# Performance work log

Measured on AMD Instinct MI355X. Metric: run time of the kernel, lower is better.

The kernel has to match this reference:

```python
import jax, jax.numpy as jnp
import numpy as np

N = 100000
E = 1600000
IN, HID, OUT = 128, 128, 64


def setup_inputs() -> dict:
    key = jax.random.key(0)
    k = jax.random.split(key, 8)
    x = jax.random.normal(k[0], (N, IN), dtype=jnp.float32)
    src = jax.random.randint(k[1], (E,), 0, N)
    dst = jax.random.randint(k[2], (E,), 0, N)
    # Glorot-ish init for the per-layer fc_neigh weights + biases
    W1 = jax.random.normal(k[3], (IN, HID), dtype=jnp.float32) / np.sqrt(IN)
    b1 = jnp.zeros((HID,), dtype=jnp.float32)
    W2 = jax.random.normal(k[4], (HID, OUT), dtype=jnp.float32) / np.sqrt(HID)
    b2 = jnp.zeros((OUT,), dtype=jnp.float32)
    return {"x": x, "src": src, "dst": dst, "W1": W1, "b1": b1, "W2": W2, "b2": b2}


def _sage_gcn_layer(h, src, dst, W, b):
    # DGL SAGEConv aggregator_type='gcn':
    #   neigh = sum_{u in N(v)} h_u ; h_neigh = (neigh + h_v) / (deg(v) + 1)
    #   out = h_neigh @ W + b   (fc_self unused for 'gcn')
    msg = h[src]                                              # [E, d] gather
    agg = jax.ops.segment_sum(msg, dst, num_segments=N)       # [N, d] scatter-add
    deg = jax.ops.segment_sum(jnp.ones((E,), h.dtype), dst, num_segments=N)
    h_neigh = (agg + h) / (deg[:, None] + 1.0)
    return h_neigh @ W + b


def reference(x, src, dst, W1, b1, W2, b2):
    # Dropout in eval mode (identity), as for a deterministic correctness baseline.
    h = _sage_gcn_layer(x, src, dst, W1, b1)
    h = jax.nn.relu(h)
    h = _sage_gcn_layer(h, src, dst, W2, b2)
    return h
```

## Files before the change

kernel.cpp:

```cpp
#include <hip/hip_runtime.h>

#define NN 100000
#define EE 1600000
#define FD 128
#define NBK 391
#define BCAP 5120
#define CHUNK 4096

typedef __attribute__((ext_vector_type(8))) short bf16x8;
typedef __attribute__((ext_vector_type(4))) float f32x4;

static __device__ __forceinline__ unsigned bfpack(float lo, float hi) {
  unsigned a = __float_as_uint(lo), b = __float_as_uint(hi);
  a = (a + 0x7FFFu + ((a >> 16) & 1u)) >> 16;
  b = (b + 0x7FFFu + ((b >> 16) & 1u)) >> 16;
  return a | (b << 16);
}
static __device__ __forceinline__ ushort bfround(float x) {
  unsigned u = __float_as_uint(x);
  u = (u + 0x7FFFu + ((u >> 16) & 1u)) >> 16;
  return (ushort)u;
}
static __device__ __forceinline__ float bflo(unsigned u) {
  return __uint_as_float(u << 16);
}
static __device__ __forceinline__ float bfhi(unsigned u) {
  return __uint_as_float(u & 0xFFFF0000u);
}

__global__ __launch_bounds__(256) void pass1_bin(const int* __restrict__ src,
                                                 const int* __restrict__ dst,
                                                 unsigned* __restrict__ gcur,
                                                 unsigned* __restrict__ arena) {
  __shared__ unsigned hist[NBK + 1];
  __shared__ unsigned scan[512];
  __shared__ unsigned gpos[NBK + 1];
  __shared__ unsigned sorted[CHUNK];
  int t = threadIdx.x;
  int base = blockIdx.x * CHUNK;

  hist[t] = 0;
  if (t + 256 <= NBK) hist[t + 256] = 0;
  __syncthreads();

  int dreg[16], sreg[16];
#pragma unroll
  for (int j = 0; j < 16; ++j) {
    int e = base + t + j * 256;
    if (e < EE) {
      dreg[j] = dst[e];
      sreg[j] = src[e];
      atomicAdd(&hist[dreg[j] >> 8], 1u);
    } else {
      dreg[j] = -1;
      sreg[j] = 0;
    }
  }
  __syncthreads();

  scan[t] = (t < NBK) ? hist[t] : 0;
  scan[t + 256] = (t + 256 < NBK) ? hist[t + 256] : 0;
  __syncthreads();
  for (int d = 1; d < 512; d <<= 1) {
    unsigned r0 = (t >= d) ? scan[t - d] : 0;
    unsigned r1 = ((t + 256) >= d) ? scan[t + 256 - d] : 0;
    __syncthreads();
    scan[t] += r0;
    scan[t + 256] += r1;
    __syncthreads();
  }
  unsigned c0 = (t < NBK) ? scan[t] - hist[t] : 0;
  unsigned c1 = (t + 256 < NBK) ? scan[t + 256] - hist[t + 256] : 0;
  __syncthreads();
  if (t < NBK) hist[t] = c0;
  if (t + 256 < NBK) hist[t + 256] = c1;
  __syncthreads();

#pragma unroll
  for (int j = 0; j < 16; ++j) {
    if (dreg[j] >= 0) {
      int b = dreg[j] >> 8;
      unsigned pos = atomicAdd(&hist[b], 1u);
      sorted[pos] = ((unsigned)(dreg[j] & 255) << 20) | (unsigned)sreg[j];
    }
  }
  __syncthreads();

  if (t < NBK) {
    unsigned lo = t ? scan[t - 1] : 0;
    unsigned cntb = scan[t] - lo;
    if (cntb) gpos[t] = atomicAdd(&gcur[t], cntb);
  }
  if (t + 256 < NBK) {
    unsigned lo = scan[t + 255];
    unsigned cntb = scan[t + 256] - lo;
    if (cntb) gpos[t + 256] = atomicAdd(&gcur[t + 256], cntb);
  }
  __syncthreads();

  int w = t >> 6, lane = t & 63;
  for (int b = w; b < NBK; b += 4) {
    unsigned lo = b ? scan[b - 1] : 0;
    unsigned cntb = scan[b] - lo;
    if (!cntb) continue;
    unsigned gp = gpos[b];
    if (gp >= BCAP) continue;
    unsigned lim = min(gp + cntb, (unsigned)BCAP) - gp;
    for (unsigned i = lane; i < lim; i += 64)
      arena[(size_t)b * BCAP + gp + i] = sorted[lo + i];
  }
}

__global__ __launch_bounds__(256) void bscan_kernel(const unsigned* __restrict__ gcur,
                                                    unsigned* __restrict__ bbase) {
  __shared__ unsigned sh[512];
  int t = threadIdx.x;
  unsigned v0 = (t < NBK) ? gcur[t] : 0;
  unsigned v1 = (t + 256 < NBK) ? gcur[t + 256] : 0;
  sh[t] = v0;
  sh[t + 256] = v1;
  __syncthreads();
  for (int d = 1; d < 512; d <<= 1) {
    unsigned r0 = (t >= d) ? sh[t - d] : 0;
    unsigned r1 = ((t + 256) >= d) ? sh[t + 256 - d] : 0;
    __syncthreads();
    sh[t] += r0;
    sh[t + 256] += r1;
    __syncthreads();
  }
  if (t < NBK) bbase[t] = sh[t] - v0;
  if (t + 256 < NBK) bbase[t + 256] = sh[t + 256] - v1;
}

__global__ __launch_bounds__(256) void pass2_sort(const unsigned* __restrict__ arena,
                                                  const unsigned* __restrict__ gcur,
                                                  const unsigned* __restrict__ bbase,
                                                  int* __restrict__ nbr,
                                                  int* __restrict__ cur) {
  __shared__ unsigned hist[256], scan[256], sorted[BCAP];
  int t = threadIdx.x;
  int b = blockIdx.x;
  unsigned cnt = min(gcur[b], (unsigned)BCAP);
  unsigned base = bbase[b];
  const unsigned* run = arena + (size_t)b * BCAP;

  hist[t] = 0;
  __syncthreads();
  for (unsigned i = t; i < cnt; i += 256) atomicAdd(&hist[run[i] >> 20], 1u);
  __syncthreads();
  scan[t] = hist[t];
  __syncthreads();
  for (int d = 1; d < 256; d <<= 1) {
    unsigned r = (t >= d) ? scan[t - d] : 0;
    __syncthreads();
    scan[t] += r;
    __syncthreads();
  }
  unsigned excl = scan[t] - hist[t];
  __syncthreads();
  hist[t] = excl;
  __syncthreads();
  for (unsigned i = t; i < cnt; i += 256) {
    unsigned v = run[i];
    unsigned pos = atomicAdd(&hist[v >> 20], 1u);
    sorted[pos] = v & 0xFFFFFu;
  }
  __syncthreads();
  for (unsigned i = t; i < cnt; i += 256) nbr[base + i] = (int)sorted[i];
  int node = b * 256 + t;
  if (node < NN) cur[node] = (int)(base + scan[t]);
}

__global__ __launch_bounds__(256) void wconv_kernel(const float* __restrict__ W,
                                                    ushort* __restrict__ Wtg,
                                                    int K, int C) {
  int i = blockIdx.x * 256 + threadIdx.x;
  if (i >= K * C) return;
  int k = i / C, c = i % C;
  Wtg[c * K + k] = bfround(W[i]);
}

template <int NCOLS, bool ABF16>
__global__ __launch_bounds__(256) void mfma_gemm(const void* __restrict__ Ap,
                                                 const ushort* __restrict__ Wtg,
                                                 ushort* __restrict__ out) {
  constexpr int NCT = NCOLS / 16;
  __shared__ ushort Wt[NCOLS * 136];
  __shared__ ushort As[64 * 136];
  int t = threadIdx.x;
  int node0 = blockIdx.x * 64;

  for (int idx = t; idx < NCOLS * 16; idx += 256) {
    int flat = idx * 8;
    int c = flat >> 7, k = flat & 127;
    uint4 v = *reinterpret_cast<const uint4*>(Wtg + flat);
    *reinterpret_cast<uint4*>(&Wt[c * 136 + k]) = v;
  }
  {
    int r = t >> 2, cq = (t & 3) * 32;
    int row = node0 + r;
    if (row >= NN) row = NN - 1;
    uint4* d = reinterpret_cast<uint4*>(&As[r * 136 + cq]);
    if constexpr (ABF16) {
      const uint4* s =
          reinterpret_cast<const uint4*>((const ushort*)Ap + (size_t)row * FD + cq);
      d[0] = s[0]; d[1] = s[1]; d[2] = s[2]; d[3] = s[3];
    } else {
      const float4* s =
          reinterpret_cast<const float4*>((const float*)Ap + (size_t)row * FD + cq);
      unsigned dv[16];
#pragma unroll
      for (int q = 0; q < 8; ++q) {
        float4 f = s[q];
        dv[q * 2 + 0] = bfpack(f.x, f.y);
        dv[q * 2 + 1] = bfpack(f.z, f.w);
      }
#pragma unroll
      for (int q = 0; q < 4; ++q)
        d[q] = make_uint4(dv[q * 4 + 0], dv[q * 4 + 1], dv[q * 4 + 2], dv[q * 4 + 3]);
    }
  }
  __syncthreads();

  int w = t >> 6;
  int l = t & 63;
  int lr = l & 15, lq = l >> 4;

  f32x4 acc[NCT];
#pragma unroll
  for (int ct = 0; ct < NCT; ++ct) acc[ct] = (f32x4)0.0f;

  const ushort* aBase = &As[(w * 16 + lr) * 136 + lq * 8];
  const ushort* bBase = &Wt[lr * 136 + lq * 8];
#pragma unroll
  for (int ks = 0; ks < 4; ++ks) {
    bf16x8 a = *reinterpret_cast<const bf16x8*>(aBase + ks * 32);
#pragma unroll
    for (int ct = 0; ct < NCT; ++ct) {
      bf16x8 b = *reinterpret_cast<const bf16x8*>(bBase + ct * 16 * 136 + ks * 32);
      acc[ct] = __builtin_amdgcn_mfma_f32_16x16x32_bf16(a, b, acc[ct], 0, 0, 0);
    }
  }

  int rowb = node0 + w * 16 + lq * 4;
#pragma unroll
  for (int ct = 0; ct < NCT; ++ct) {
#pragma unroll
    for (int r = 0; r < 4; ++r) {
      int row = rowb + r;
      if (row < NN) out[(size_t)row * NCOLS + ct * 16 + lr] = bfround(acc[ct][r]);
    }
  }
}

__global__ __launch_bounds__(256) void gather128_kernel(const unsigned* __restrict__ Y,
                                                        const int* __restrict__ cur,
                                                        const int* __restrict__ nbr,
                                                        const float* __restrict__ bias,
                                                        unsigned* __restrict__ outp) {
  int w = (blockIdx.x * 256 + threadIdx.x) >> 6;
  if (w >= NN) return;
  int lane = threadIdx.x & 63;
  int s0 = __builtin_amdgcn_readfirstlane(w ? cur[w - 1] : 0);
  int s1 = __builtin_amdgcn_readfirstlane(cur[w]);
  float inv = 1.0f / (float)(s1 - s0 + 1);
  float ax = 0.f, ay = 0.f;
  int j = s0;
  for (; j + 4 <= s1; j += 4) {
    unsigned a = Y[(size_t)nbr[j] * 64 + lane];
    unsigned b = Y[(size_t)nbr[j + 1] * 64 + lane];
    unsigned c = Y[(size_t)nbr[j + 2] * 64 + lane];
    unsigned d = Y[(size_t)nbr[j + 3] * 64 + lane];
    ax += (bflo(a) + bflo(b)) + (bflo(c) + bflo(d));
    ay += (bfhi(a) + bfhi(b)) + (bfhi(c) + bfhi(d));
  }
  for (; j < s1; ++j) {
    unsigned a = Y[(size_t)nbr[j] * 64 + lane];
    ax += bflo(a);
    ay += bfhi(a);
  }
  unsigned sv = Y[(size_t)w * 64 + lane];
  float2 bv = reinterpret_cast<const float2*>(bias)[lane];
  float rx = fmaxf((ax + bflo(sv)) * inv + bv.x, 0.f);
  float ry = fmaxf((ay + bfhi(sv)) * inv + bv.y, 0.f);
  outp[(size_t)w * 64 + lane] = bfpack(rx, ry);
}

__global__ __launch_bounds__(256) void gather64_kernel(const ushort* __restrict__ Y,
                                                       const int* __restrict__ cur,
                                                       const int* __restrict__ nbr,
                                                       const float* __restrict__ bias,
                                                       float* __restrict__ out) {
  int w = (blockIdx.x * 256 + threadIdx.x) >> 6;
  if (w >= NN) return;
  int lane = threadIdx.x & 63;
  int s0 = __builtin_amdgcn_readfirstlane(w ? cur[w - 1] : 0);
  int s1 = __builtin_amdgcn_readfirstlane(cur[w]);
  float inv = 1.0f / (float)(s1 - s0 + 1);
  float acc = 0.f;
  int j = s0;
  for (; j + 4 <= s1; j += 4) {
    float a = __uint_as_float((unsigned)Y[(size_t)nbr[j] * 64 + lane] << 16);
    float b = __uint_as_float((unsigned)Y[(size_t)nbr[j + 1] * 64 + lane] << 16);
    float c = __uint_as_float((unsigned)Y[(size_t)nbr[j + 2] * 64 + lane] << 16);
    float d = __uint_as_float((unsigned)Y[(size_t)nbr[j + 3] * 64 + lane] << 16);
    acc += (a + b) + (c + d);
  }
  for (; j < s1; ++j)
    acc += __uint_as_float((unsigned)Y[(size_t)nbr[j] * 64 + lane] << 16);
  float self = __uint_as_float((unsigned)Y[(size_t)w * 64 + lane] << 16);
  out[(size_t)w * 64 + lane] = (acc + self) * inv + bias[lane];
}

extern "C" void kernel_launch(void* const* d_in, const int* in_sizes, int n_in,
                              void* d_out, int out_size, void* d_ws, size_t ws_size,
                              hipStream_t stream) {
  const float* x  = (const float*)d_in[0];
  const int* src  = (const int*)d_in[1];
  const int* dst  = (const int*)d_in[2];
  const float* W1 = (const float*)d_in[3];
  const float* b1 = (const float*)d_in[4];
  const float* W2 = (const float*)d_in[5];
  const float* b2 = (const float*)d_in[6];
  float* out = (float*)d_out;

  char* ws = (char*)d_ws;
  ushort*   Wt1g  = (ushort*)(ws + 0);
  ushort*   Wt2g  = (ushort*)(ws + 32768);
  unsigned* gcur  = (unsigned*)(ws + 49152);
  unsigned* bbase = (unsigned*)(ws + 51200);
  int*      cur   = (int*)(ws + 53248);
  int*      nbr   = (int*)(ws + 453248);
  unsigned* arena = (unsigned*)(ws + 6853248);
  ushort*   ybuf  = (ushort*)(ws + 14860928);
  ushort*   h1    = (ushort*)(ws + 40460928);

  const int gemmBlocks = (NN + 63) / 64;
  const int gathBlocks = NN / 4;

  hipMemsetAsync(gcur, 0, NBK * sizeof(unsigned), stream);
  pass1_bin<<<NBK, 256, 0, stream>>>(src, dst, gcur, arena);
  bscan_kernel<<<1, 256, 0, stream>>>(gcur, bbase);
  wconv_kernel<<<64, 256, 0, stream>>>(W1, Wt1g, 128, 128);
  wconv_kernel<<<32, 256, 0, stream>>>(W2, Wt2g, 128, 64);
  pass2_sort<<<NBK, 256, 0, stream>>>(arena, gcur, bbase, nbr, cur);

  mfma_gemm<128, false><<<gemmBlocks, 256, 0, stream>>>(x, Wt1g, ybuf);
  gather128_kernel<<<gathBlocks, 256, 0, stream>>>((const unsigned*)ybuf, cur, nbr, b1,
                                                   (unsigned*)h1);

  mfma_gemm<64, true><<<gemmBlocks, 256, 0, stream>>>(h1, Wt2g, ybuf);
  gather64_kernel<<<gathBlocks, 256, 0, stream>>>(ybuf, cur, nbr, b2, out);
}
```

Measured before the change: 209.5 us.

## Fold bucket scan into sort, merge weight conversions, gather two nodes per wave

Removes the single-block bucket scan kernel by having every pass2_sort block redundantly compute the 391-entry prefix sum in shared memory, and merges the two weight-conversion launches into one, cutting launch count and serialization. Both gather kernels now process two destination nodes per wavefront with interleaved loads, doubling independent memory requests in flight to hide gather latency. The cost is higher register pressure and some imbalance when the two nodes have different degrees.

```diff
diff --git a/kernel.cpp b/kernel.cpp
--- a/kernel.cpp
+++ b/kernel.cpp
@@ -111,10 +111,15 @@
   }
 }
 
-__global__ __launch_bounds__(256) void bscan_kernel(const unsigned* __restrict__ gcur,
-                                                    unsigned* __restrict__ bbase) {
+__global__ __launch_bounds__(256) void pass2_sort(const unsigned* __restrict__ arena,
+                                                  const unsigned* __restrict__ gcur,
+                                                  int* __restrict__ nbr,
+                                                  int* __restrict__ cur) {
   __shared__ unsigned sh[512];
+  __shared__ unsigned hist[256], scn[256], sorted[BCAP];
   int t = threadIdx.x;
+  int b = blockIdx.x;
+
   unsigned v0 = (t < NBK) ? gcur[t] : 0;
   unsigned v1 = (t + 256 < NBK) ? gcur[t + 256] : 0;
   sh[t] = v0;
@@ -128,35 +133,23 @@
     sh[t + 256] += r1;
     __syncthreads();
   }
-  if (t < NBK) bbase[t] = sh[t] - v0;
-  if (t + 256 < NBK) bbase[t + 256] = sh[t + 256] - v1;
-}
-
-__global__ __launch_bounds__(256) void pass2_sort(const unsigned* __restrict__ arena,
-                                                  const unsigned* __restrict__ gcur,
-                                                  const unsigned* __restrict__ bbase,
-                                                  int* __restrict__ nbr,
-                                                  int* __restrict__ cur) {
-  __shared__ unsigned hist[256], scan[256], sorted[BCAP];
-  int t = threadIdx.x;
-  int b = blockIdx.x;
-  unsigned cnt = min(gcur[b], (unsigned)BCAP);
-  unsigned base = bbase[b];
+  unsigned base = b ? sh[b - 1] : 0;
+  unsigned cnt = min(sh[b] - base, (unsigned)BCAP);
   const unsigned* run = arena + (size_t)b * BCAP;
 
   hist[t] = 0;
   __syncthreads();
   for (unsigned i = t; i < cnt; i += 256) atomicAdd(&hist[run[i] >> 20], 1u);
   __syncthreads();
-  scan[t] = hist[t];
+  scn[t] = hist[t];
   __syncthreads();
   for (int d = 1; d < 256; d <<= 1) {
-    unsigned r = (t >= d) ? scan[t - d] : 0;
-    __syncthreads();
-    scan[t] += r;
-    __syncthreads();
-  }
-  unsigned excl = scan[t] - hist[t];
+    unsigned r = (t >= d) ? scn[t - d] : 0;
+    __syncthreads();
+    scn[t] += r;
+    __syncthreads();
+  }
+  unsigned excl = scn[t] - hist[t];
   __syncthreads();
   hist[t] = excl;
   __syncthreads();
@@ -168,16 +161,24 @@
   __syncthreads();
   for (unsigned i = t; i < cnt; i += 256) nbr[base + i] = (int)sorted[i];
   int node = b * 256 + t;
-  if (node < NN) cur[node] = (int)(base + scan[t]);
-}
-
-__global__ __launch_bounds__(256) void wconv_kernel(const float* __restrict__ W,
-                                                    ushort* __restrict__ Wtg,
-                                                    int K, int C) {
+  if (node < NN) cur[node] = (int)(base + scn[t]);
+}
+
+__global__ __launch_bounds__(256) void wconv_kernel(const float* __restrict__ W1,
+                                                    const float* __restrict__ W2,
+                                                    ushort* __restrict__ Wt1g,
+                                                    ushort* __restrict__ Wt2g) {
   int i = blockIdx.x * 256 + threadIdx.x;
-  if (i >= K * C) return;
-  int k = i / C, c = i % C;
-  Wtg[c * K + k] = bfround(W[i]);
+  if (i < 128 * 128) {
+    int k = i >> 7, c = i & 127;
+    Wt1g[c * 128 + k] = bfround(W1[i]);
+  } else {
+    int j = i - 128 * 128;
+    if (j < 128 * 64) {
+      int k = j / 64, c = j % 64;
+      Wt2g[c * 128 + k] = bfround(W2[j]);
+    }
+  }
 }
 
 template <int NCOLS, bool ABF16>
@@ -258,32 +259,71 @@
                                                         const int* __restrict__ nbr,
                                                         const float* __restrict__ bias,
                                                         unsigned* __restrict__ outp) {
-  int w = (blockIdx.x * 256 + threadIdx.x) >> 6;
-  if (w >= NN) return;
+  int wv = (blockIdx.x * 256 + threadIdx.x) >> 6;
+  int v0 = wv * 2;
+  if (v0 >= NN) return;
+  int v1 = v0 + 1;
   int lane = threadIdx.x & 63;
-  int s0 = __builtin_amdgcn_readfirstlane(w ? cur[w - 1] : 0);
-  int s1 = __builtin_amdgcn_readfirstlane(cur[w]);
-  float inv = 1.0f / (float)(s1 - s0 + 1);
-  float ax = 0.f, ay = 0.f;
-  int j = s0;
-  for (; j + 4 <= s1; j += 4) {
-    unsigned a = Y[(size_t)nbr[j] * 64 + lane];
-    unsigned b = Y[(size_t)nbr[j + 1] * 64 + lane];
-    unsigned c = Y[(size_t)nbr[j + 2] * 64 + lane];
-    unsigned d = Y[(size_t)nbr[j + 3] * 64 + lane];
-    ax += (bflo(a) + bflo(b)) + (bflo(c) + bflo(d));
-    ay += (bfhi(a) + bfhi(b)) + (bfhi(c) + bfhi(d));
-  }
-  for (; j < s1; ++j) {
-    unsigned a = Y[(size_t)nbr[j] * 64 + lane];
-    ax += bflo(a);
-    ay += bfhi(a);
-  }
-  unsigned sv = Y[(size_t)w * 64 + lane];
+  int e0a = __builtin_amdgcn_readfirstlane(v0 ? cur[v0 - 1] : 0);
+  int e1a = __builtin_amdgcn_readfirstlane(cur[v0]);
+  int e1b = __builtin_amdgcn_readfirstlane(cur[v1]);
+  int e0b = e1a;
+  float invA = 1.0f / (float)(e1a - e0a + 1);
+  float invB = 1.0f / (float)(e1b - e0b + 1);
+
+  float ax0 = 0.f, ay0 = 0.f, ax1 = 0.f, ay1 = 0.f;
+  int ja = e0a, jb = e0b;
+  while (ja + 4 <= e1a && jb + 4 <= e1b) {
+    unsigned a0 = Y[(size_t)nbr[ja + 0] * 64 + lane];
+    unsigned a1 = Y[(size_t)nbr[ja + 1] * 64 + lane];
+    unsigned a2 = Y[(size_t)nbr[ja + 2] * 64 + lane];
+    unsigned a3 = Y[(size_t)nbr[ja + 3] * 64 + lane];
+    unsigned b0 = Y[(size_t)nbr[jb + 0] * 64 + lane];
+    unsigned b1 = Y[(size_t)nbr[jb + 1] * 64 + lane];
+    unsigned b2 = Y[(size_t)nbr[jb + 2] * 64 + lane];
+    unsigned b3 = Y[(size_t)nbr[jb + 3] * 64 + lane];
+    ax0 += (bflo(a0) + bflo(a1)) + (bflo(a2) + bflo(a3));
+    ay0 += (bfhi(a0) + bfhi(a1)) + (bfhi(a2) + bfhi(a3));
+    ax1 += (bflo(b0) + bflo(b1)) + (bflo(b2) + bflo(b3));
+    ay1 += (bfhi(b0) + bfhi(b1)) + (bfhi(b2) + bfhi(b3));
+    ja += 4;
+    jb += 4;
+  }
+  for (; ja + 4 <= e1a; ja += 4) {
+    unsigned a0 = Y[(size_t)nbr[ja + 0] * 64 + lane];
+    unsigned a1 = Y[(size_t)nbr[ja + 1] * 64 + lane];
+    unsigned a2 = Y[(size_t)nbr[ja + 2] * 64 + lane];
+    unsigned a3 = Y[(size_t)nbr[ja + 3] * 64 + lane];
+    ax0 += (bflo(a0) + bflo(a1)) + (bflo(a2) + bflo(a3));
+    ay0 += (bfhi(a0) + bfhi(a1)) + (bfhi(a2) + bfhi(a3));
+  }
+  for (; jb + 4 <= e1b; jb += 4) {
+    unsigned b0 = Y[(size_t)nbr[jb + 0] * 64 + lane];
+    unsigned b1 = Y[(size_t)nbr[jb + 1] * 64 + lane];
+    unsigned b2 = Y[(size_t)nbr[jb + 2] * 64 + lane];
+    unsigned b3 = Y[(size_t)nbr[jb + 3] * 64 + lane];
+    ax1 += (bflo(b0) + bflo(b1)) + (bflo(b2) + bflo(b3));
+    ay1 += (bfhi(b0) + bfhi(b1)) + (bfhi(b2) + bfhi(b3));
+  }
+  for (; ja < e1a; ++ja) {
+    unsigned a = Y[(size_t)nbr[ja] * 64 + lane];
+    ax0 += bflo(a);
+    ay0 += bfhi(a);
+  }
+  for (; jb < e1b; ++jb) {
+    unsigned b = Y[(size_t)nbr[jb] * 64 + lane];
+    ax1 += bflo(b);
+    ay1 += bfhi(b);
+  }
+  unsigned sv0 = Y[(size_t)v0 * 64 + lane];
+  unsigned sv1 = Y[(size_t)v1 * 64 + lane];
   float2 bv = reinterpret_cast<const float2*>(bias)[lane];
-  float rx = fmaxf((ax + bflo(sv)) * inv + bv.x, 0.f);
-  float ry = fmaxf((ay + bfhi(sv)) * inv + bv.y, 0.f);
-  outp[(size_t)w * 64 + lane] = bfpack(rx, ry);
+  float rx0 = fmaxf((ax0 + bflo(sv0)) * invA + bv.x, 0.f);
+  float ry0 = fmaxf((ay0 + bfhi(sv0)) * invA + bv.y, 0.f);
+  float rx1 = fmaxf((ax1 + bflo(sv1)) * invB + bv.x, 0.f);
+  float ry1 = fmaxf((ay1 + bfhi(sv1)) * invB + bv.y, 0.f);
+  outp[(size_t)v0 * 64 + lane] = bfpack(rx0, ry0);
+  outp[(size_t)v1 * 64 + lane] = bfpack(rx1, ry1);
 }
 
 __global__ __launch_bounds__(256) void gather64_kernel(const ushort* __restrict__ Y,
@@ -291,25 +331,58 @@
                                                        const int* __restrict__ nbr,
                                                        const float* __restrict__ bias,
                                                        float* __restrict__ out) {
-  int w = (blockIdx.x * 256 + threadIdx.x) >> 6;
-  if (w >= NN) return;
+  int wv = (blockIdx.x * 256 + threadIdx.x) >> 6;
+  int v0 = wv * 2;
+  if (v0 >= NN) return;
+  int v1 = v0 + 1;
   int lane = threadIdx.x & 63;
-  int s0 = __builtin_amdgcn_readfirstlane(w ? cur[w - 1] : 0);
-  int s1 = __builtin_amdgcn_readfirstlane(cur[w]);
-  float inv = 1.0f / (float)(s1 - s0 + 1);
-  float acc = 0.f;
-  int j = s0;
-  for (; j + 4 <= s1; j += 4) {
-    float a = __uint_as_float((unsigned)Y[(size_t)nbr[j] * 64 + lane] << 16);
-    float b = __uint_as_float((unsigned)Y[(size_t)nbr[j + 1] * 64 + lane] << 16);
-    float c = __uint_as_float((unsigned)Y[(size_t)nbr[j + 2] * 64 + lane] << 16);
-    float d = __uint_as_float((unsigned)Y[(size_t)nbr[j + 3] * 64 + lane] << 16);
-    acc += (a + b) + (c + d);
-  }
-  for (; j < s1; ++j)
-    acc += __uint_as_float((unsigned)Y[(size_t)nbr[j] * 64 + lane] << 16);
-  float self = __uint_as_float((unsigned)Y[(size_t)w * 64 + lane] << 16);
-  out[(size_t)w * 64 + lane] = (acc + self) * inv + bias[lane];
+  int e0a = __builtin_amdgcn_readfirstlane(v0 ? cur[v0 - 1] : 0);
+  int e1a = __builtin_amdgcn_readfirstlane(cur[v0]);
+  int e1b = __builtin_amdgcn_readfirstlane(cur[v1]);
+  int e0b = e1a;
+  float invA = 1.0f / (float)(e1a - e0a + 1);
+  float invB = 1.0f / (float)(e1b - e0b + 1);
+
+  float s0 = 0.f, s1 = 0.f;
+  int ja = e0a, jb = e0b;
+  while (ja + 4 <= e1a && jb + 4 <= e1b) {
+    float a0 = __uint_as_float((unsigned)Y[(size_t)nbr[ja + 0] * 64 + lane] << 16);
+    float a1 = __uint_as_float((unsigned)Y[(size_t)nbr[ja + 1] * 64 + lane] << 16);
+    float a2 = __uint_as_float((unsigned)Y[(size_t)nbr[ja + 2] * 64 + lane] << 16);
+    float a3 = __uint_as_float((unsigned)Y[(size_t)nbr[ja + 3] * 64 + lane] << 16);
+    float b0 = __uint_as_float((unsigned)Y[(size_t)nbr[jb + 0] * 64 + lane] << 16);
+    float b1 = __uint_as_float((unsigned)Y[(size_t)nbr[jb + 1] * 64 + lane] << 16);
+    float b2 = __uint_as_float((unsigned)Y[(size_t)nbr[jb + 2] * 64 + lane] << 16);
+    float b3 = __uint_as_float((unsigned)Y[(size_t)nbr[jb + 3] * 64 + lane] << 16);
+    s0 += (a0 + a1) + (a2 + a3);
+    s1 += (b0 + b1) + (b2 + b3);
+    ja += 4;
+    jb += 4;
+  }
+  for (; ja + 4 <= e1a; ja += 4) {
+    float a0 = __uint_as_float((unsigned)Y[(size_t)nbr[ja + 0] * 64 + lane] << 16);
+    float a1 = __uint_as_float((unsigned)Y[(size_t)nbr[ja + 1] * 64 + lane] << 16);
+    float a2 = __uint_as_float((unsigned)Y[(size_t)nbr[ja + 2] * 64 + lane] << 16);
+    float a3 = __uint_as_float((unsigned)Y[(size_t)nbr[ja + 3] * 64 + lane] << 16);
+    s0 += (a0 + a1) + (a2 + a3);
+  }
+  for (; jb + 4 <= e1b; jb += 4) {
+    float b0 = __uint_as_float((unsigned)Y[(size_t)nbr[jb + 0] * 64 + lane] << 16);
+    float b1 = __uint_as_float((unsigned)Y[(size_t)nbr[jb + 1] * 64 + lane] << 16);
+    float b2 = __uint_as_float((unsigned)Y[(size_t)nbr[jb + 2] * 64 + lane] << 16);
+    float b3 = __uint_as_float((unsigned)Y[(size_t)nbr[jb + 3] * 64 + lane] << 16);
+    s1 += (b0 + b1) + (b2 + b3);
+  }
+  for (; ja < e1a; ++ja)
+    s0 += __uint_as_float((unsigned)Y[(size_t)nbr[ja] * 64 + lane] << 16);
+  for (; jb < e1b; ++jb)
+    s1 += __uint_as_float((unsigned)Y[(size_t)nbr[jb] * 64 + lane] << 16);
+
+  float self0 = __uint_as_float((unsigned)Y[(size_t)v0 * 64 + lane] << 16);
+  float self1 = __uint_as_float((unsigned)Y[(size_t)v1 * 64 + lane] << 16);
+  float bvv = bias[lane];
+  out[(size_t)v0 * 64 + lane] = (s0 + self0) * invA + bvv;
+  out[(size_t)v1 * 64 + lane] = (s1 + self1) * invB + bvv;
 }
 
 extern "C" void kernel_launch(void* const* d_in, const int* in_sizes, int n_in,
@@ -328,7 +401,6 @@
   ushort*   Wt1g  = (ushort*)(ws + 0);
   ushort*   Wt2g  = (ushort*)(ws + 32768);
   unsigned* gcur  = (unsigned*)(ws + 49152);
-  unsigned* bbase = (unsigned*)(ws + 51200);
   int*      cur   = (int*)(ws + 53248);
   int*      nbr   = (int*)(ws + 453248);
   unsigned* arena = (unsigned*)(ws + 6853248);
@@ -336,14 +408,12 @@
   ushort*   h1    = (ushort*)(ws + 40460928);
 
   const int gemmBlocks = (NN + 63) / 64;
-  const int gathBlocks = NN / 4;
+  const int gathBlocks = (NN / 2 + 3) / 4;
 
   hipMemsetAsync(gcur, 0, NBK * sizeof(unsigned), stream);
   pass1_bin<<<NBK, 256, 0, stream>>>(src, dst, gcur, arena);
-  bscan_kernel<<<1, 256, 0, stream>>>(gcur, bbase);
-  wconv_kernel<<<64, 256, 0, stream>>>(W1, Wt1g, 128, 128);
-  wconv_kernel<<<32, 256, 0, stream>>>(W2, Wt2g, 128, 64);
-  pass2_sort<<<NBK, 256, 0, stream>>>(arena, gcur, bbase, nbr, cur);
+  wconv_kernel<<<96, 256, 0, stream>>>(W1, W2, Wt1g, Wt2g);
+  pass2_sort<<<NBK, 256, 0, stream>>>(arena, gcur, nbr, cur);
 
   mfma_gemm<128, false><<<gemmBlocks, 256, 0, stream>>>(x, Wt1g, ybuf);
   gather128_kernel<<<gathBlocks, 256, 0, stream>>>((const unsigned*)ybuf, cur, nbr, b1,
```

Measured after the change: 194.5 us. -7.1%, faster.
